# Kernel tuning notes

Measured on AMD Instinct MI355X. Metric: run time of the kernel, lower is better.

The kernel has to match this reference:

```python
import jax, jax.numpy as jnp
import numpy as np

DIM, DIM_KQ, DIM_V, N = 1024, 64, 64, 8192

def setup_inputs() -> dict:
    key = jax.random.key(0)
    kx, kq, kk, kv = jax.random.split(key, 4)
    x = jax.random.normal(kx, (N, DIM), dtype=jnp.float32)
    # original uses torch.rand (uniform [0,1)) for parameter init
    w_q = jax.random.uniform(kq, (DIM, DIM_KQ), dtype=jnp.float32)
    w_k = jax.random.uniform(kk, (DIM, DIM_KQ), dtype=jnp.float32)
    w_v = jax.random.uniform(kv, (DIM, DIM_V), dtype=jnp.float32)
    return {"x": x, "w_q": w_q, "w_k": w_k, "w_v": w_v}

def reference(x, w_q, w_k, w_v):
    q = x @ w_q            # [N, dkq]
    k = x @ w_k            # [N, dkq]
    v = x @ w_v            # [N, dv]
    scale = 1.0 / jnp.sqrt(jnp.asarray(DIM_KQ, dtype=x.dtype))
    att_s = (q @ k.T) * scale           # [N, N]
    att_w = jax.nn.softmax(att_s, axis=-1)
    return att_w @ v                    # [N, dv]
```

## Files before the change

### kernel.cpp

```cpp
#include <hip/hip_runtime.h>
#include <hip/hip_bf16.h>
#include <math.h>

constexpr int N    = 8192;
constexpr int DIM  = 1024;

typedef __attribute__((ext_vector_type(8))) short bf16x8;
typedef __attribute__((ext_vector_type(4))) float f32x4;

__device__ inline unsigned short f2bf(float f) {
    unsigned u = __float_as_uint(f);
    u += 0x7fffu + ((u >> 16) & 1u);
    return (unsigned short)(u >> 16);
}
__device__ inline float bf2f(unsigned short h) {
    return __uint_as_float((unsigned)h << 16);
}
__device__ inline unsigned cvtpk(float a, float b) {
    unsigned r;
    asm("v_cvt_pk_bf16_f32 %0, %1, %2" : "=v"(r) : "v"(a), "v"(b));
    return r;
}
__device__ inline void gload16(const void* gsrc, void* ldst) {
    typedef __attribute__((address_space(1))) const unsigned int GU;
    typedef __attribute__((address_space(3))) unsigned int LU;
    __builtin_amdgcn_global_load_lds((GU*)gsrc, (LU*)ldst, 16, 0, 0);
}

__global__ __launch_bounds__(256) void prep_w_kernel(
    const float* __restrict__ wq, const float* __restrict__ wk,
    const float* __restrict__ wv,
    unsigned short* __restrict__ wthi, unsigned short* __restrict__ wtlo)
{
    int idx = blockIdx.x * 256 + threadIdx.x;
    int c   = idx >> 10;
    int k   = idx & 1023;
    const float* wsrc = (c < 64) ? wq : (c < 128) ? wk : wv;
    float f = wsrc[(size_t)k * 64 + (c & 63)];
    unsigned short h = f2bf(f);
    int pos = c * 1024 + (k & ~63) + ((((k >> 3) & 7) ^ (c & 7)) << 3) + (k & 7);
    wthi[pos] = h;
    wtlo[pos] = f2bf(f - bf2f(h));
}

__global__ __launch_bounds__(256) void proj_kernel(
    const float* __restrict__ x,
    const unsigned short* __restrict__ wthi,
    const unsigned short* __restrict__ wtlo,
    unsigned short* __restrict__ qhi, unsigned short* __restrict__ qlo,
    unsigned short* __restrict__ khi, unsigned short* __restrict__ klo,
    unsigned short* __restrict__ vthi)
{
    __shared__ unsigned short As[2][2][4096];
    __shared__ unsigned short Bs[2][2][3072];

    const int tid  = threadIdx.x;
    const int lane = tid & 63;
    const int w    = tid >> 6;
    const int g16  = lane >> 4;
    const int i16  = lane & 15;
    const int row0 = blockIdx.x * 64;
    const int col0 = blockIdx.y * 48;

    float4 xn[2][4];
    auto loadX = [&](int t, int s) {
#pragma unroll
        for (int i = 0; i < 4; ++i) {
            int f4 = i * 256 + tid;
            xn[s][i] = *reinterpret_cast<const float4*>(
                x + (size_t)(row0 + (f4 >> 4)) * DIM + t * 64 + (f4 & 15) * 4);
        }
    };
    auto stageB = [&](int t, int buf) {
#pragma unroll
        for (int i = 0; i < 3; ++i) {
            int idx = i * 256 + tid;
            int p   = (idx >= 384) ? 1 : 0;
            int li  = idx - p * 384;
            const unsigned short* base = p ? wtlo : wthi;
            const unsigned short* src  = base + (size_t)(col0 + (li >> 3)) * 1024
                                         + t * 64 + (li & 7) * 8;
            gload16(src, (char*)&Bs[buf][p][0] + (size_t)li * 16);
        }
    };
    auto writeA = [&](int buf, int s) {
#pragma unroll
        for (int i = 0; i < 4; ++i) {
            int f4 = i * 256 + tid;
            int r = f4 >> 4, c4 = f4 & 15;
            float4 v = xn[s][i];
            unsigned h01 = cvtpk(v.x, v.y);
            unsigned h23 = cvtpk(v.z, v.w);
            float hx = __uint_as_float(h01 << 16);
            float hy = __uint_as_float(h01 & 0xffff0000u);
            float hz = __uint_as_float(h23 << 16);
            float hw = __uint_as_float(h23 & 0xffff0000u);
            uint2 uh = { h01, h23 };
            uint2 ul = { cvtpk(v.x - hx, v.y - hy), cvtpk(v.z - hz, v.w - hw) };
            int byte = r * 128 + (((c4 >> 1) ^ (r & 7)) << 4) + ((c4 & 1) << 3);
            *reinterpret_cast<uint2*>((char*)&As[buf][0][0] + byte) = uh;
            *reinterpret_cast<uint2*>((char*)&As[buf][1][0] + byte) = ul;
        }
    };

    f32x4 acc[3];
    acc[0] = acc[1] = acc[2] = (f32x4){0.f, 0.f, 0.f, 0.f};

    loadX(0, 0);
    loadX(1, 1);
    stageB(0, 0);
    writeA(0, 0);

    const int arow = w * 16 + i16;
#pragma unroll
    for (int t = 0; t < 16; ++t) {
        const int b = t & 1;
        __syncthreads();
        if (t < 15) stageB(t + 1, b ^ 1);
        if (t < 14) loadX(t + 2, b);
        bf16x8 ah[2], al[2];
#pragma unroll
        for (int kc = 0; kc < 2; ++kc) {
            int off = arow * 128 + ((((kc << 2) | g16) ^ (arow & 7)) << 4);
            ah[kc] = *reinterpret_cast<const bf16x8*>((char*)&As[b][0][0] + off);
            al[kc] = *reinterpret_cast<const bf16x8*>((char*)&As[b][1][0] + off);
        }
#pragma unroll
        for (int ct = 0; ct < 3; ++ct) {
            const int colL = ct * 16 + i16;
#pragma unroll
            for (int kc = 0; kc < 2; ++kc) {
                int off = colL * 128 + ((((kc << 2) | g16) ^ (colL & 7)) << 4);
                bf16x8 bh = *reinterpret_cast<const bf16x8*>((char*)&Bs[b][0][0] + off);
                bf16x8 bl = *reinterpret_cast<const bf16x8*>((char*)&Bs[b][1][0] + off);
                acc[ct] = __builtin_amdgcn_mfma_f32_16x16x32_bf16(ah[kc], bh, acc[ct], 0, 0, 0);
                acc[ct] = __builtin_amdgcn_mfma_f32_16x16x32_bf16(ah[kc], bl, acc[ct], 0, 0, 0);
                acc[ct] = __builtin_amdgcn_mfma_f32_16x16x32_bf16(al[kc], bh, acc[ct], 0, 0, 0);
            }
        }
        if (t < 15) writeA(b ^ 1, b ^ 1);
    }

    const float QSCALE = 0.180336880f;
#pragma unroll
    for (int ct = 0; ct < 3; ++ct) {
        int cglob = col0 + ct * 16 + i16;
        int g = cglob >> 6, c64 = cglob & 63;
#pragma unroll
        for (int rr = 0; rr < 4; ++rr) {
            int row = row0 + w * 16 + 4 * g16 + rr;
            float f = acc[ct][rr];
            if (g == 0) {
                f *= QSCALE;
                unsigned short h = f2bf(f);
                qhi[(size_t)row * 64 + c64] = h;
                qlo[(size_t)row * 64 + c64] = f2bf(f - bf2f(h));
            } else if (g == 1) {
                int ci = c64 ^ ((row & 7) << 3);
                unsigned short h = f2bf(f);
                khi[(size_t)row * 64 + ci] = h;
                klo[(size_t)row * 64 + ci] = f2bf(f - bf2f(h));
            } else {
                int cg  = row >> 3;
                int cgs = (cg & ~7) | ((cg & 7) ^ (c64 & 7));
                vthi[(size_t)c64 * 8192 + cgs * 8 + (row & 7)] = f2bf(f);
            }
        }
    }
}

constexpr int BQ = 128;
constexpr int BK = 64;

__global__ __launch_bounds__(256) void attn_kernel(
    const unsigned short* __restrict__ qhi, const unsigned short* __restrict__ qlo,
    const unsigned short* __restrict__ khi, const unsigned short* __restrict__ klo,
    const unsigned short* __restrict__ vthi,
    float* __restrict__ po, float* __restrict__ pm, float* __restrict__ pl,
    int keys_per_split)
{
    __shared__ __align__(16) unsigned short stage[2][12288];
    __shared__ __align__(16) unsigned short plds[4][2][1024];

    const int tid  = threadIdx.x;
    const int lane = tid & 63;
    const int w    = tid >> 6;
    const int g16  = lane >> 4;
    const int i16  = lane & 15;
    const int qrow0 = blockIdx.x * BQ;
    const int split = blockIdx.y;
    const int key0  = split * keys_per_split;
    const int nt    = keys_per_split / BK;
    const int xorm  = (i16 & 7) << 4;
    const int wbase = i16 * 128;

    bf16x8 qh[2][2], ql[2][2];
#pragma unroll
    for (int s = 0; s < 2; ++s) {
        const size_t qr = (size_t)(qrow0 + w * 32 + s * 16 + i16) * 64;
#pragma unroll
        for (int c = 0; c < 2; ++c) {
            qh[s][c] = *reinterpret_cast<const bf16x8*>(qhi + qr + c * 32 + g16 * 8);
            ql[s][c] = *reinterpret_cast<const bf16x8*>(qlo + qr + c * 32 + g16 * 8);
        }
    }
    bf16x8 ones;
#pragma unroll
    for (int e = 0; e < 8; ++e) ones[e] = (short)0x3F80;

    float m[2] = {-INFINITY, -INFINITY};
    f32x4 o_acc[2][4], o5[2];
#pragma unroll
    for (int s = 0; s < 2; ++s) {
        o5[s] = {0.f, 0.f, 0.f, 0.f};
#pragma unroll
        for (int db = 0; db < 4; ++db) o_acc[s][db] = {0.f, 0.f, 0.f, 0.f};
    }

    auto stageKV = [&](int t, int buf) {
        const int key0t = key0 + t * BK;
#pragma unroll
        for (int u = 0; u < 6; ++u) {
            int row = ((u & 1) << 5) + (tid >> 3);
            int ch  = tid & 7;
            const unsigned short* src;
            if (u < 2)      src = khi  + (size_t)(key0t + row) * 64 + ch * 8;
            else if (u < 4) src = klo  + (size_t)(key0t + row) * 64 + ch * 8;
            else            src = vthi + (size_t)row * 8192 + key0t + ch * 8;
            gload16(src, (char*)&stage[buf][0] + u * 4096 + tid * 16);
        }
    };

    stageKV(0, 0);

    for (int t = 0; t < nt; ++t) {
        const int b = t & 1;
        __syncthreads();
        if (t + 1 < nt) stageKV(t + 1, b ^ 1);
        const char* stg = (const char*)&stage[b][0];

        f32x4 sacc[2][4];
#pragma unroll
        for (int j = 0; j < 4; ++j) {
            sacc[0][j] = {0.f, 0.f, 0.f, 0.f};
            sacc[1][j] = {0.f, 0.f, 0.f, 0.f};
        }
#pragma unroll
        for (int c = 0; c < 2; ++c) {
            bf16x8 kh[4], kl[4];
#pragma unroll
            for (int j = 0; j < 4; ++j) {
                const int kr = 16 * j + i16;
                const int byteO = kr * 128 + ((c * 64 + g16 * 16) ^ ((kr & 7) << 4));
                kh[j] = *reinterpret_cast<const bf16x8*>(stg + byteO);
                kl[j] = *reinterpret_cast<const bf16x8*>(stg + byteO + 8192);
            }
#pragma unroll
            for (int j = 0; j < 4; ++j)
#pragma unroll
                for (int s = 0; s < 2; ++s)
                    sacc[s][j] = __builtin_amdgcn_mfma_f32_16x16x32_bf16(
                                     kh[j], qh[s][c], sacc[s][j], 0, 0, 0);
#pragma unroll
            for (int j = 0; j < 4; ++j)
#pragma unroll
                for (int s = 0; s < 2; ++s)
                    sacc[s][j] = __builtin_amdgcn_mfma_f32_16x16x32_bf16(
                                     kh[j], ql[s][c], sacc[s][j], 0, 0, 0);
#pragma unroll
            for (int j = 0; j < 4; ++j)
#pragma unroll
                for (int s = 0; s < 2; ++s)
                    sacc[s][j] = __builtin_amdgcn_mfma_f32_16x16x32_bf16(
                                     kl[j], qh[s][c], sacc[s][j], 0, 0, 0);
        }

        float aloc[2];
#pragma unroll
        for (int s = 0; s < 2; ++s) {
            float a0 = fmaxf(fmaxf(sacc[s][0][0], sacc[s][0][1]), fmaxf(sacc[s][0][2], sacc[s][0][3]));
            float a1 = fmaxf(fmaxf(sacc[s][1][0], sacc[s][1][1]), fmaxf(sacc[s][1][2], sacc[s][1][3]));
            float a2 = fmaxf(fmaxf(sacc[s][2][0], sacc[s][2][1]), fmaxf(sacc[s][2][2], sacc[s][2][3]));
            float a3 = fmaxf(fmaxf(sacc[s][3][0], sacc[s][3][1]), fmaxf(sacc[s][3][2], sacc[s][3][3]));
            aloc[s] = fmaxf(fmaxf(a0, a1), fmaxf(a2, a3));
        }
        int need = (aloc[0] > m[0] + 8.f) | (aloc[1] > m[1] + 8.f);
        if (__any(need)) {
#pragma unroll
            for (int s = 0; s < 2; ++s) {
                float x2 = fmaxf(aloc[s], __shfl_xor(aloc[s], 16));
                x2 = fmaxf(x2, __shfl_xor(x2, 32));
                float mn   = fmaxf(m[s], x2);
                float corr = exp2f(m[s] - mn);
                m[s] = mn;
                o5[s] *= corr;
#pragma unroll
                for (int db = 0; db < 4; ++db) o_acc[s][db] *= corr;
            }
        }

        bf16x8 pfrag[2][2];
#pragma unroll
        for (int s = 0; s < 2; ++s) {
            char* pb = (char*)&plds[w][s][0];
#pragma unroll
            for (int j = 0; j < 4; ++j) {
                float p0 = exp2f(sacc[s][j][0] - m[s]);
                float p1 = exp2f(sacc[s][j][1] - m[s]);
                float p2 = exp2f(sacc[s][j][2] - m[s]);
                float p3 = exp2f(sacc[s][j][3] - m[s]);
                uint2 pdw = { cvtpk(p0, p1), cvtpk(p2, p3) };
                *reinterpret_cast<uint2*>(pb + wbase + ((32 * j + 8 * g16) ^ xorm)) = pdw;
            }
#pragma unroll
            for (int c = 0; c < 2; ++c)
                pfrag[s][c] = *reinterpret_cast<const bf16x8*>(
                    pb + wbase + ((64 * c + 16 * g16) ^ xorm));
        }

#pragma unroll
        for (int c = 0; c < 2; ++c) {
            bf16x8 vh[4];
#pragma unroll
            for (int db = 0; db < 4; ++db) {
                const int vr = 16 * db + i16;
                const int byteO = 16384 + vr * 128 +
                                  ((c * 64 + g16 * 16) ^ ((vr & 7) << 4));
                vh[db] = *reinterpret_cast<const bf16x8*>(stg + byteO);
            }
            o5[0] = __builtin_amdgcn_mfma_f32_16x16x32_bf16(ones, pfrag[0][c], o5[0], 0, 0, 0);
            o5[1] = __builtin_amdgcn_mfma_f32_16x16x32_bf16(ones, pfrag[1][c], o5[1], 0, 0, 0);
#pragma unroll
            for (int db = 0; db < 4; ++db)
#pragma unroll
                for (int s = 0; s < 2; ++s)
                    o_acc[s][db] = __builtin_amdgcn_mfma_f32_16x16x32_bf16(
                                       vh[db], pfrag[s][c], o_acc[s][db], 0, 0, 0);
        }
    }

#pragma unroll
    for (int s = 0; s < 2; ++s) {
        const size_t prow = (size_t)split * N + qrow0 + w * 32 + s * 16;
#pragma unroll
        for (int db = 0; db < 4; ++db) {
            float4 ov = {o_acc[s][db][0], o_acc[s][db][1],
                         o_acc[s][db][2], o_acc[s][db][3]};
            *reinterpret_cast<float4*>(po + (prow + i16) * 64 + 16 * db + 4 * g16) = ov;
        }
        if (lane < 16) {
            pm[prow + i16] = m[s];
            pl[prow + i16] = o5[s][0];
        }
    }
}

__global__ __launch_bounds__(256) void combine_kernel(
    const float* __restrict__ po,
    const float* __restrict__ pm,
    const float* __restrict__ pl,
    float* __restrict__ out, int ns)
{
    const int tid = threadIdx.x;
    const int row = blockIdx.x * 16 + (tid >> 4);
    const int c4  = tid & 15;

    float M = -INFINITY;
    for (int s = 0; s < ns; ++s)
        M = fmaxf(M, pm[(size_t)s * N + row]);
    float L = 0.f;
    float4 acc = {0.f, 0.f, 0.f, 0.f};
    for (int s = 0; s < ns; ++s) {
        float ws = exp2f(pm[(size_t)s * N + row] - M);
        L += ws * pl[(size_t)s * N + row];
        float4 ov = *reinterpret_cast<const float4*>(
            po + ((size_t)s * N + row) * 64 + c4 * 4);
        acc.x += ws * ov.x; acc.y += ws * ov.y;
        acc.z += ws * ov.z; acc.w += ws * ov.w;
    }
    float inv = 1.f / L;
    float4 res = {acc.x * inv, acc.y * inv, acc.z * inv, acc.w * inv};
    *reinterpret_cast<float4*>(out + (size_t)row * 64 + c4 * 4) = res;
}

extern "C" void kernel_launch(void* const* d_in, const int* in_sizes, int n_in,
                              void* d_out, int out_size, void* d_ws, size_t ws_size,
                              hipStream_t stream)
{
    const float* x  = (const float*)d_in[0];
    const float* wq = (const float*)d_in[1];
    const float* wk = (const float*)d_in[2];
    const float* wv = (const float*)d_in[3];
    float* out = (float*)d_out;

    const size_t PLANE = (size_t)N * 64;
    unsigned short* qhi  = (unsigned short*)d_ws;
    unsigned short* qlo  = qhi + PLANE;
    unsigned short* khi  = qlo + PLANE;
    unsigned short* klo  = khi + PLANE;
    unsigned short* vthi = klo + PLANE;
    const size_t plane_bytes = 5 * PLANE * 2;
    const size_t wt_elems = (size_t)192 * 1024;
    const size_t wt_bytes = 2 * wt_elems * 2;

    int ns = 8;
    while (ns > 1 &&
           plane_bytes + wt_bytes +
           (size_t)ns * ((size_t)N * 64 * 4 + (size_t)N * 8) > ws_size)
        ns >>= 1;

    float* po = (float*)((char*)d_ws + plane_bytes);
    float* pm = po + (size_t)ns * N * 64;
    float* pl = pm + (size_t)ns * N;
    unsigned short* wthi = (unsigned short*)(pl + (size_t)ns * N);
    unsigned short* wtlo = wthi + wt_elems;

    prep_w_kernel<<<768, 256, 0, stream>>>(wq, wk, wv, wthi, wtlo);

    dim3 pgrid(N / 64, 4);
    proj_kernel<<<pgrid, 256, 0, stream>>>(x, wthi, wtlo,
                                           qhi, qlo, khi, klo, vthi);

    dim3 agrid(N / BQ, ns);
    attn_kernel<<<agrid, 256, 0, stream>>>(qhi, qlo, khi, klo, vthi,
                                           po, pm, pl, N / ns);

    combine_kernel<<<N / 16, 256, 0, stream>>>(po, pm, pl, out, ns);
}
```

Measured before the change: 84.88 us.

## Retile projection kernel to 32-row by 64-column blocks aligned to q/k/v

```diff
diff --git a/kernel.cpp b/kernel.cpp
--- a/kernel.cpp
+++ b/kernel.cpp
@@ -51,21 +51,21 @@
     unsigned short* __restrict__ khi, unsigned short* __restrict__ klo,
     unsigned short* __restrict__ vthi)
 {
-    __shared__ unsigned short As[2][2][4096];
-    __shared__ unsigned short Bs[2][2][3072];
+    __shared__ unsigned short As[2][2][2048];
+    __shared__ unsigned short Bs[2][2][4096];
 
     const int tid  = threadIdx.x;
     const int lane = tid & 63;
     const int w    = tid >> 6;
     const int g16  = lane >> 4;
     const int i16  = lane & 15;
-    const int row0 = blockIdx.x * 64;
-    const int col0 = blockIdx.y * 48;
-
-    float4 xn[2][4];
+    const int row0 = blockIdx.x * 32;
+    const int col0 = blockIdx.y * 64;
+
+    float4 xn[2][2];
     auto loadX = [&](int t, int s) {
 #pragma unroll
-        for (int i = 0; i < 4; ++i) {
+        for (int i = 0; i < 2; ++i) {
             int f4 = i * 256 + tid;
             xn[s][i] = *reinterpret_cast<const float4*>(
                 x + (size_t)(row0 + (f4 >> 4)) * DIM + t * 64 + (f4 & 15) * 4);
@@ -73,10 +73,10 @@
     };
     auto stageB = [&](int t, int buf) {
 #pragma unroll
-        for (int i = 0; i < 3; ++i) {
+        for (int i = 0; i < 4; ++i) {
             int idx = i * 256 + tid;
-            int p   = (idx >= 384) ? 1 : 0;
-            int li  = idx - p * 384;
+            int p   = idx >> 9;
+            int li  = idx & 511;
             const unsigned short* base = p ? wtlo : wthi;
             const unsigned short* src  = base + (size_t)(col0 + (li >> 3)) * 1024
                                          + t * 64 + (li & 7) * 8;
@@ -85,7 +85,7 @@
     };
     auto writeA = [&](int buf, int s) {
 #pragma unroll
-        for (int i = 0; i < 4; ++i) {
+        for (int i = 0; i < 2; ++i) {
             int f4 = i * 256 + tid;
             int r = f4 >> 4, c4 = f4 & 15;
             float4 v = xn[s][i];
@@ -103,53 +103,58 @@
         }
     };
 
-    f32x4 acc[3];
-    acc[0] = acc[1] = acc[2] = (f32x4){0.f, 0.f, 0.f, 0.f};
+    f32x4 acc[2];
+    acc[0] = acc[1] = (f32x4){0.f, 0.f, 0.f, 0.f};
 
     loadX(0, 0);
     loadX(1, 1);
     stageB(0, 0);
     writeA(0, 0);
 
-    const int arow = w * 16 + i16;
+    const int colL = w * 16 + i16;
 #pragma unroll
     for (int t = 0; t < 16; ++t) {
         const int b = t & 1;
         __syncthreads();
         if (t < 15) stageB(t + 1, b ^ 1);
         if (t < 14) loadX(t + 2, b);
-        bf16x8 ah[2], al[2];
+        bf16x8 ah[2][2], al[2][2];
+#pragma unroll
+        for (int rt = 0; rt < 2; ++rt)
+#pragma unroll
+            for (int kc = 0; kc < 2; ++kc) {
+                int arow = rt * 16 + i16;
+                int off = arow * 128 + ((((kc << 2) | g16) ^ (arow & 7)) << 4);
+                ah[rt][kc] = *reinterpret_cast<const bf16x8*>((char*)&As[b][0][0] + off);
+                al[rt][kc] = *reinterpret_cast<const bf16x8*>((char*)&As[b][1][0] + off);
+            }
 #pragma unroll
         for (int kc = 0; kc < 2; ++kc) {
-            int off = arow * 128 + ((((kc << 2) | g16) ^ (arow & 7)) << 4);
-            ah[kc] = *reinterpret_cast<const bf16x8*>((char*)&As[b][0][0] + off);
-            al[kc] = *reinterpret_cast<const bf16x8*>((char*)&As[b][1][0] + off);
-        }
-#pragma unroll
-        for (int ct = 0; ct < 3; ++ct) {
-            const int colL = ct * 16 + i16;
-#pragma unroll
-            for (int kc = 0; kc < 2; ++kc) {
-                int off = colL * 128 + ((((kc << 2) | g16) ^ (colL & 7)) << 4);
-                bf16x8 bh = *reinterpret_cast<const bf16x8*>((char*)&Bs[b][0][0] + off);
-                bf16x8 bl = *reinterpret_cast<const bf16x8*>((char*)&Bs[b][1][0] + off);
-                acc[ct] = __builtin_amdgcn_mfma_f32_16x16x32_bf16(ah[kc], bh, acc[ct], 0, 0, 0);
-                acc[ct] = __builtin_amdgcn_mfma_f32_16x16x32_bf16(ah[kc], bl, acc[ct], 0, 0, 0);
-                acc[ct] = __builtin_amdgcn_mfma_f32_16x16x32_bf16(al[kc], bh, acc[ct], 0, 0, 0);
-            }
+            int off = colL * 128 + ((((kc << 2) | g16) ^ (colL & 7)) << 4);
+            bf16x8 bh = *reinterpret_cast<const bf16x8*>((char*)&Bs[b][0][0] + off);
+            bf16x8 bl = *reinterpret_cast<const bf16x8*>((char*)&Bs[b][1][0] + off);
+#pragma unroll
+            for (int rt = 0; rt < 2; ++rt)
+                acc[rt] = __builtin_amdgcn_mfma_f32_16x16x32_bf16(ah[rt][kc], bh, acc[rt], 0, 0, 0);
+#pragma unroll
+            for (int rt = 0; rt < 2; ++rt)
+                acc[rt] = __builtin_amdgcn_mfma_f32_16x16x32_bf16(ah[rt][kc], bl, acc[rt], 0, 0, 0);
+#pragma unroll
+            for (int rt = 0; rt < 2; ++rt)
+                acc[rt] = __builtin_amdgcn_mfma_f32_16x16x32_bf16(al[rt][kc], bh, acc[rt], 0, 0, 0);
         }
         if (t < 15) writeA(b ^ 1, b ^ 1);
     }
 
     const float QSCALE = 0.180336880f;
-#pragma unroll
-    for (int ct = 0; ct < 3; ++ct) {
-        int cglob = col0 + ct * 16 + i16;
-        int g = cglob >> 6, c64 = cglob & 63;
+    const int cglob = col0 + w * 16 + i16;
+    const int g = cglob >> 6, c64 = cglob & 63;
+#pragma unroll
+    for (int rt = 0; rt < 2; ++rt)
 #pragma unroll
         for (int rr = 0; rr < 4; ++rr) {
-            int row = row0 + w * 16 + 4 * g16 + rr;
-            float f = acc[ct][rr];
+            int row = row0 + rt * 16 + 4 * g16 + rr;
+            float f = acc[rt][rr];
             if (g == 0) {
                 f *= QSCALE;
                 unsigned short h = f2bf(f);
@@ -166,7 +171,6 @@
                 vthi[(size_t)c64 * 8192 + cgs * 8 + (row & 7)] = f2bf(f);
             }
         }
-    }
 }
 
 constexpr int BQ = 128;
@@ -417,7 +421,7 @@
 
     prep_w_kernel<<<768, 256, 0, stream>>>(wq, wk, wv, wthi, wtlo);
 
-    dim3 pgrid(N / 64, 4);
+    dim3 pgrid(N / 32, 3);
     proj_kernel<<<pgrid, 256, 0, stream>>>(x, wthi, wtlo,
                                            qhi, qlo, khi, klo, vthi);
 
```

Result: no change. 84.34 us (-0.6%).
